# Kernel optimization log

Measured on AMD Instinct MI355X. Metric: run time of the kernel, lower is better.

## Reference

```python
import jax, jax.numpy as jnp
import numpy as np
import math

ALPHA = 2.0  # spikingjelly surrogate.ATan default alpha
TAU = 2.0
MEM_DECAY = math.exp(-1.0 / TAU)
ADAPT_STRENGTH = 0.1
TARGET_RATE = 0.02
THR_MIN = 0.5
N_HEAD = 4

@jax.custom_vjp
def spike_fn(x):
    # Heaviside forward, ATan surrogate backward
    return (x >= 0.0).astype(x.dtype)

def _spike_fwd(x):
    return spike_fn(x), x

def _spike_bwd(x, g):
    return (g * (ALPHA / 2.0) / (1.0 + (jnp.pi / 2.0 * ALPHA * x) ** 2),)

spike_fn.defvjp(_spike_fwd, _spike_bwd)

def lif_step(x, v_mem, thr):
    # thr is a buffer in torch (updated under no_grad): no grad flows to it
    thr_c = jax.lax.stop_gradient(thr)
    v_pot = v_mem * MEM_DECAY + x
    spike = spike_fn(v_pot - thr_c)
    v_new = v_pot * (1.0 - jax.lax.stop_gradient(spike))
    err = jax.lax.stop_gradient(jnp.mean(spike)) - TARGET_RATE
    thr_new = jnp.maximum(thr_c + ADAPT_STRENGTH * err, THR_MIN)
    return spike, v_new, thr_new

def setup_inputs() -> dict:
    key = jax.random.key(0)
    ks = jax.random.split(key, 10)
    B, T, S, D, DS = 8, 16, 256, 512, 64
    x = jax.random.normal(ks[0], (B, T, S, D), jnp.float32)
    A = jax.random.normal(ks[1], (DS, DS), jnp.float32)
    C = jax.random.normal(ks[2], (D, DS), jnp.float32)
    s = 1.0 / math.sqrt(DS)
    Wq = jax.random.uniform(ks[3], (DS, DS), jnp.float32, -s, s)
    bq = jax.random.uniform(ks[4], (DS,), jnp.float32, -s, s)
    sd = 1.0 / math.sqrt(D)
    Wkv = jax.random.uniform(ks[5], (2 * DS, D), jnp.float32, -sd, sd)
    bkv = jax.random.uniform(ks[6], (2 * DS,), jnp.float32, -sd, sd)
    Wo = jax.random.uniform(ks[7], (DS, DS), jnp.float32, -s, s)
    bo = jax.random.uniform(ks[8], (DS,), jnp.float32, -s, s)
    thr_s0 = jnp.full((DS,), 1.0, jnp.float32)
    thr_o0 = jnp.full((D,), 1.0, jnp.float32)
    return {"x": x, "A": A, "C": C, "Wq": Wq, "bq": bq, "Wkv": Wkv,
            "bkv": bkv, "Wo": Wo, "bo": bo, "thr_s0": thr_s0, "thr_o0": thr_o0}

def reference(x, A, C, Wq, bq, Wkv, bkv, Wo, bo, thr_s0, thr_o0):
    B, T, S, D = x.shape
    DS = A.shape[0]
    H = N_HEAD
    dh = DS // H
    N = B * S
    scale = 1.0 / math.sqrt(dh)
    h0 = jnp.zeros((B, S, DS), x.dtype)
    sv0 = jnp.zeros((B, S, DS), x.dtype)
    ov0 = jnp.zeros((B, S, D), x.dtype)

    def step(carry, x_t):
        h, sv, ov, ts, to = carry
        state_transition = h @ A.T                              # (B,S,DS)
        q = (h @ Wq.T + bq).reshape(N, H, dh).transpose(1, 0, 2)   # (H,N,dh)
        kv = x_t @ Wkv.T + bkv                                  # (B,S,2*DS)
        k = kv[..., :DS].reshape(N, H, dh).transpose(1, 0, 2)   # (H,N,dh)
        v = kv[..., DS:].reshape(N, H, dh).transpose(1, 0, 2)   # (H,N,dh)
        scores = jnp.einsum('hnd,hmd->hnm', q, k) * scale       # (H,N,N)
        w = jax.nn.softmax(scores, axis=-1)
        att = jnp.einsum('hnm,hmd->hnd', w, v)                  # (H,N,dh)
        att = att.transpose(1, 0, 2).reshape(B, S, DS)
        state_update = state_transition + att @ Wo.T + bo
        h2, sv2, ts2 = lif_step(state_update, sv, ts)
        output_potential = h2 @ C.T                             # (B,S,D)
        out, ov2, to2 = lif_step(output_potential, ov, to)
        return (h2, sv2, ov2, ts2, to2), out

    _, outs = jax.lax.scan(step, (h0, sv0, ov0, thr_s0, thr_o0),
                           jnp.moveaxis(x, 1, 0))               # outs: (T,B,S,D)
    return jnp.moveaxis(outs, 0, 1)                             # (B,T,S,D)
```

## Files before the change

### kernel.cpp

```cpp
#include <hip/hip_runtime.h>
#include <math.h>


#define NTOK   2048
#define TSTEPS 16
#define NSPLIT 32

#define MEMDECAY ((float)0.6065306597126334)
#define SCALE    0.25f
#define LOG2E    1.4426950408889634f

#define OFF_KV   ((size_t)0)
#define OFF_PACC ((size_t)4194304)
#define OFF_OV   ((size_t)8388608)
#define OFF_H    ((size_t)9437184)
#define OFF_SV   ((size_t)9568256)
#define OFF_Q    ((size_t)9699328)
#define OFF_PM   ((size_t)9830400)
#define OFF_PL   ((size_t)10092544)
#define OFF_CT   ((size_t)10354688)
#define OFF_CNT  ((size_t)10387456)
#define OFF_WT   ((size_t)10387488)
#define OFF_HM   ((size_t)10453024)

__global__ __launch_bounds__(256) void init_kernel(const float* __restrict__ bq,
                                                   const float* __restrict__ C,
                                                   const float* __restrict__ Wkv,
                                                   float* __restrict__ ws) {
  int i = blockIdx.x * 256 + threadIdx.x;
  if (i < 327680) {
    float4 z = {0.f, 0.f, 0.f, 0.f};
    ((float4*)(ws + OFF_OV))[i] = z;
    return;
  }
  i -= 327680;
  if (i < 131072) { ws[OFF_Q + i] = bq[i & 63]; return; }
  i -= 131072;
  if (i < 32768) {
    int k = i >> 9, c = i & 511;
    ws[OFF_CT + i] = C[c * 64 + k];
    return;
  }
  i -= 32768;
  if (i < 65536) {
    int k = i >> 7, o = i & 127;
    ws[OFF_WT + i] = Wkv[o * 512 + k];
    return;
  }
  i -= 65536;
  if (i < 32) { ((int*)(ws + OFF_CNT))[i] = 0; return; }
  i -= 32;
  if (i < 1024) {
    float4 z = {0.f, 0.f, 0.f, 0.f};
    ((float4*)(ws + OFF_HM))[i] = z;
  }
}

__global__ __launch_bounds__(256) void kv_gemm_kernel(const float* __restrict__ x,
                                                      const float* __restrict__ wkt,
                                                      const float* __restrict__ bkv,
                                                      float* __restrict__ ws) {
  __shared__ float xs[64 * 68];
  __shared__ float wt[64 * 136];
  const int tid = threadIdx.x;
  const int mbase = blockIdx.x * 64;
  const int rg = tid >> 4;
  const int cg = tid & 15;

  float acc[4][8];
#pragma unroll
  for (int i = 0; i < 4; ++i)
#pragma unroll
    for (int j = 0; j < 8; ++j) acc[i][j] = 0.f;

  for (int kt = 0; kt < 8; ++kt) {
    const int kb = kt * 64;
#pragma unroll
    for (int p = 0; p < 4; ++p) {
      int e = tid + p * 256;
      int r = e >> 4, kq = e & 15;
      int row = mbase + r;
      int t_ = row >> 11, n = row & 2047;
      int b = n >> 8, s = n & 255;
      float4 v = *(const float4*)(x + (size_t)((b * 16 + t_) * 256 + s) * 512 + kb + kq * 4);
      *(float4*)(xs + r * 68 + kq * 4) = v;
    }
#pragma unroll
    for (int p = 0; p < 8; ++p) {
      int e = tid + p * 256;
      int k = e >> 5, cq = e & 31;
      float4 v = *(const float4*)(wkt + (size_t)(kb + k) * 128 + cq * 4);
      *(float4*)(wt + k * 136 + cq * 4) = v;
    }
    __syncthreads();
#pragma unroll 2
    for (int kq = 0; kq < 16; ++kq) {
      float4 a0 = *(const float4*)(xs + (rg * 4 + 0) * 68 + kq * 4);
      float4 a1 = *(const float4*)(xs + (rg * 4 + 1) * 68 + kq * 4);
      float4 a2 = *(const float4*)(xs + (rg * 4 + 2) * 68 + kq * 4);
      float4 a3 = *(const float4*)(xs + (rg * 4 + 3) * 68 + kq * 4);
      const float* ap[4] = {(const float*)&a0, (const float*)&a1,
                            (const float*)&a2, (const float*)&a3};
#pragma unroll
      for (int kk = 0; kk < 4; ++kk) {
        const float* wp = wt + (kq * 4 + kk) * 136;
        float4 b0 = *(const float4*)(wp + cg * 4);
        float4 b1 = *(const float4*)(wp + 64 + cg * 4);
#pragma unroll
        for (int i = 0; i < 4; ++i) {
          float av = ap[i][kk];
          acc[i][0] += av * b0.x; acc[i][1] += av * b0.y;
          acc[i][2] += av * b0.z; acc[i][3] += av * b0.w;
          acc[i][4] += av * b1.x; acc[i][5] += av * b1.y;
          acc[i][6] += av * b1.z; acc[i][7] += av * b1.w;
        }
      }
    }
    __syncthreads();
  }
  float4 bb0 = *(const float4*)(bkv + cg * 4);
  float4 bb1 = *(const float4*)(bkv + 64 + cg * 4);
  float* kvout = ws + OFF_KV;
#pragma unroll
  for (int i = 0; i < 4; ++i) {
    float* op = kvout + (size_t)(mbase + rg * 4 + i) * 128;
    float4 v0; v0.x = acc[i][0] + bb0.x; v0.y = acc[i][1] + bb0.y;
    v0.z = acc[i][2] + bb0.z; v0.w = acc[i][3] + bb0.w;
    float4 v1; v1.x = acc[i][4] + bb1.x; v1.y = acc[i][5] + bb1.y;
    v1.z = acc[i][6] + bb1.z; v1.w = acc[i][7] + bb1.w;
    *(float4*)(op + cg * 4) = v0;
    *(float4*)(op + 64 + cg * 4) = v1;
  }
}

__device__ __forceinline__ void attp_body(int blk, int tid, int t,
                                          const float* __restrict__ kvbase,
                                          const float* __restrict__ qbuf,
                                          float* __restrict__ pm,
                                          float* __restrict__ pl,
                                          float* __restrict__ pacc,
                                          float* smem) {
  const int head = blk & 3;
  const int qt = (blk >> 2) & 3;
  const int sp = blk >> 4;
  float* kl = smem;
  float* vl = smem + 1024;
  const float* kvt = kvbase + (size_t)t * NTOK * 128;
  {
    int key = tid >> 2, dq = tid & 3;
    const float* base = kvt + (size_t)(sp * 64 + key) * 128 + head * 16;
    float4 kk = ((const float4*)base)[dq];
    float4 vv = ((const float4*)(base + 64))[dq];
    ((float4*)kl)[key * 4 + dq] = kk;
    ((float4*)vl)[key * 4 + dq] = vv;
  }
  const int i0 = qt * 512 + tid;
  const int i1 = i0 + 256;
  float q0[16], q1[16];
  {
    const float4* qp0 = (const float4*)(qbuf + (size_t)i0 * 64 + head * 16);
    const float4* qp1 = (const float4*)(qbuf + (size_t)i1 * 64 + head * 16);
#pragma unroll
    for (int r = 0; r < 4; ++r) {
      float4 a = qp0[r];
      q0[4 * r] = a.x; q0[4 * r + 1] = a.y; q0[4 * r + 2] = a.z; q0[4 * r + 3] = a.w;
      float4 b = qp1[r];
      q1[4 * r] = b.x; q1[4 * r + 1] = b.y; q1[4 * r + 2] = b.z; q1[4 * r + 3] = b.w;
    }
  }
  __syncthreads();
  float m0 = -INFINITY, l0 = 0.f, m1 = -INFINITY, l1 = 0.f;
  float acc0[16], acc1[16];
#pragma unroll
  for (int d = 0; d < 16; ++d) { acc0[d] = 0.f; acc1[d] = 0.f; }

#pragma unroll
  for (int ch = 0; ch < 4; ++ch) {
    float sc0[16], sc1[16];
#pragma unroll
    for (int j = 0; j < 16; ++j) {
      const float* kp = kl + (ch * 16 + j) * 16;
      float s0 = 0.f, s1 = 0.f;
#pragma unroll
      for (int d = 0; d < 16; ++d) { float kv_ = kp[d]; s0 += q0[d] * kv_; s1 += q1[d] * kv_; }
      sc0[j] = s0 * SCALE; sc1[j] = s1 * SCALE;
    }
    float mb0 = sc0[0], mb1 = sc1[0];
#pragma unroll
    for (int j = 1; j < 16; ++j) { mb0 = fmaxf(mb0, sc0[j]); mb1 = fmaxf(mb1, sc1[j]); }
    float mn0 = fmaxf(m0, mb0), mn1 = fmaxf(m1, mb1);
    float r0 = exp2f((m0 - mn0) * LOG2E), r1 = exp2f((m1 - mn1) * LOG2E);
    l0 *= r0; l1 *= r1;
#pragma unroll
    for (int d = 0; d < 16; ++d) { acc0[d] *= r0; acc1[d] *= r1; }
#pragma unroll
    for (int j = 0; j < 16; ++j) {
      float w0 = exp2f((sc0[j] - mn0) * LOG2E), w1 = exp2f((sc1[j] - mn1) * LOG2E);
      l0 += w0; l1 += w1; sc0[j] = w0; sc1[j] = w1;
    }
#pragma unroll
    for (int j = 0; j < 16; ++j) {
      const float* vp = vl + (ch * 16 + j) * 16;
      float w0 = sc0[j], w1 = sc1[j];
#pragma unroll
      for (int d = 0; d < 16; ++d) { float vv = vp[d]; acc0[d] += w0 * vv; acc1[d] += w1 * vv; }
    }
    m0 = mn0; m1 = mn1;
  }
  const int pbase = (head * NSPLIT + sp) * NTOK;
  pm[pbase + i0] = m0; pm[pbase + i1] = m1;
  pl[pbase + i0] = l0; pl[pbase + i1] = l1;
  float4* pa0 = (float4*)(pacc + (size_t)(pbase + i0) * 16);
  float4* pa1 = (float4*)(pacc + (size_t)(pbase + i1) * 16);
#pragma unroll
  for (int r = 0; r < 4; ++r) {
    float4 v0; v0.x = acc0[4 * r]; v0.y = acc0[4 * r + 1]; v0.z = acc0[4 * r + 2]; v0.w = acc0[4 * r + 3];
    pa0[r] = v0;
    float4 v1; v1.x = acc1[4 * r]; v1.y = acc1[4 * r + 1]; v1.z = acc1[4 * r + 2]; v1.w = acc1[4 * r + 3];
    pa1[r] = v1;
  }
}

__global__ __launch_bounds__(256) void attp_kernel(int t, float* __restrict__ ws) {
  __shared__ float smem[2048];
  attp_body(blockIdx.x, threadIdx.x, t, ws + OFF_KV, ws + OFF_Q,
            ws + OFF_PM, ws + OFF_PL, ws + OFF_PACC, smem);
}

__global__ __launch_bounds__(256) void combine_lifs_kernel(
    int t, const float* __restrict__ A, const float* __restrict__ Wq,
    const float* __restrict__ bq, const float* __restrict__ Wo,
    const float* __restrict__ bo, const float* __restrict__ thr_s0,
    float* __restrict__ ws) {
  __shared__ float As[64 * 68], Wqs[64 * 68], Wos[64 * 68];
  __shared__ float att_s[4][64];
  __shared__ int scnt;
  const int tid = threadIdx.x;
#pragma unroll
  for (int p = 0; p < 4; ++p) {
    int e = tid + p * 256;
    int c = e >> 4, kq = e & 15;
    *(float4*)(As + c * 68 + kq * 4)  = *(const float4*)(A + c * 64 + kq * 4);
    *(float4*)(Wqs + c * 68 + kq * 4) = *(const float4*)(Wq + c * 64 + kq * 4);
    *(float4*)(Wos + c * 68 + kq * 4) = *(const float4*)(Wo + c * 64 + kq * 4);
  }
  if (tid == 0) scnt = 0;

  const float* pm = ws + OFF_PM;
  const float* pl = ws + OFF_PL;
  const float* pacc = ws + OFF_PACC;
  float* sv = ws + OFF_SV;
  float* qb = ws + OFF_Q;
  int* cnt = (int*)(ws + OFF_CNT);
  unsigned long long* hmask = (unsigned long long*)(ws + OFF_HM);

  const int lane = tid & 63, w = tid >> 6;
  const int n = blockIdx.x * 4 + w;
  const int head = lane >> 4, d = lane & 15;
  const int pb = head * NSPLIT * NTOK + n;

  float mstar = -INFINITY;
  for (int s = 0; s < NSPLIT; ++s) mstar = fmaxf(mstar, pm[pb + s * NTOK]);
  float lst = 0.f, av = 0.f;
  for (int s = 0; s < NSPLIT; ++s) {
    float e = exp2f((pm[pb + s * NTOK] - mstar) * LOG2E);
    lst += e * pl[pb + s * NTOK];
    av += e * pacc[(size_t)(pb + s * NTOK) * 16 + d];
  }
  att_s[w][lane] = av / lst;
  unsigned long long hm = hmask[n];
  __syncthreads();

  float st = 0.f;
  {
    unsigned long long m = hm;
    while (m) {
      int k = __builtin_ctzll(m);
      m &= m - 1;
      st += As[lane * 68 + k];
    }
  }
  const float* Wor = Wos + lane * 68;
  float wo = 0.f;
#pragma unroll
  for (int kq = 0; kq < 16; ++kq) {
    float4 wb = *(const float4*)(Wor + kq * 4);
    float4 ab = *(const float4*)(&att_s[w][kq * 4]);
    wo += ab.x * wb.x; wo += ab.y * wb.y; wo += ab.z * wb.z; wo += ab.w * wb.w;
  }
  float su = st + wo + bo[lane];

  float thr = thr_s0[0];
  const float inv = 1.0f / 131072.0f;
  for (int i = 0; i < t; ++i) {
    float mean = (float)cnt[i] * inv;
    thr = fmaxf(thr + 0.1f * (mean - 0.02f), 0.5f);
  }
  float svo = sv[n * 64 + lane];
  float vpot = svo * MEMDECAY + su;
  float spk = (vpot >= thr) ? 1.f : 0.f;
  sv[n * 64 + lane] = vpot * (1.f - spk);
  unsigned long long sm = __ballot(spk > 0.5f);

  float qv = 0.f;
  {
    unsigned long long m = sm;
    while (m) {
      int k = __builtin_ctzll(m);
      m &= m - 1;
      qv += Wqs[lane * 68 + k];
    }
  }
  qb[n * 64 + lane] = qv + bq[lane];

  if (lane == 0) {
    hmask[n] = sm;
    atomicAdd(&scnt, __popcll(sm));
  }
  __syncthreads();
  if (tid == 0) atomicAdd(&cnt[t], scnt);
}

__global__ __launch_bounds__(256) void fused_out_attp_kernel(
    int t, const float* __restrict__ thr_o0, float* __restrict__ out,
    float* __restrict__ ws) {
  __shared__ float smem[2048];
  __shared__ int scnt;
  const int blk = blockIdx.x;
  if (blk >= 256) {
    attp_body(blk - 256, threadIdx.x, t + 1, ws + OFF_KV, ws + OFF_Q,
              ws + OFF_PM, ws + OFF_PL, ws + OFF_PACC, smem);
    return;
  }
  const int tid = threadIdx.x;
  const int nt = blk >> 3;
  const int ct = blk & 7;
  const float* Ct = ws + OFF_CT;
  float* ov = ws + OFF_OV;
  int* cnt = (int*)(ws + OFF_CNT);
  const unsigned long long* hmask = (const unsigned long long*)(ws + OFF_HM);

  if (tid == 0) scnt = 0;
  __syncthreads();

  const int tr = tid >> 4, tc = tid & 15;
  float thr = thr_o0[0];
  const float inv = 1.0f / 1048576.0f;
  for (int i = 0; i < t; ++i) {
    float mean = (float)cnt[16 + i] * inv;
    thr = fmaxf(thr + 0.1f * (mean - 0.02f), 0.5f);
  }

  int mycount = 0;
#pragma unroll
  for (int i = 0; i < 4; ++i) {
    int n = nt * 64 + tr + i * 16;
    size_t coff = (size_t)ct * 64 + tc * 4;
    float a0 = 0.f, a1 = 0.f, a2 = 0.f, a3 = 0.f;
    unsigned long long m = hmask[n];
    while (m) {
      int k = __builtin_ctzll(m);
      m &= m - 1;
      float4 c = *(const float4*)(Ct + (size_t)k * 512 + coff);
      a0 += c.x; a1 += c.y; a2 += c.z; a3 += c.w;
    }
    int b = n >> 8, s = n & 255;
    float* ovp = ov + (size_t)n * 512 + coff;
    float* outp = out + ((size_t)(b * 16 + t) * 256 + s) * 512 + coff;
    float4 o = *(float4*)ovp;
    float v0 = o.x * MEMDECAY + a0;
    float v1 = o.y * MEMDECAY + a1;
    float v2 = o.z * MEMDECAY + a2;
    float v3 = o.w * MEMDECAY + a3;
    float s0 = (v0 >= thr) ? 1.f : 0.f;
    float s1 = (v1 >= thr) ? 1.f : 0.f;
    float s2 = (v2 >= thr) ? 1.f : 0.f;
    float s3 = (v3 >= thr) ? 1.f : 0.f;
    float4 sp; sp.x = s0; sp.y = s1; sp.z = s2; sp.w = s3;
    *(float4*)outp = sp;
    float4 nv; nv.x = v0 * (1.f - s0); nv.y = v1 * (1.f - s1);
    nv.z = v2 * (1.f - s2); nv.w = v3 * (1.f - s3);
    *(float4*)ovp = nv;
    mycount += (int)(s0 + s1 + s2 + s3);
  }
  atomicAdd(&scnt, mycount);
  __syncthreads();
  if (tid == 0) atomicAdd(&cnt[16 + t], scnt);
}

extern "C" void kernel_launch(void* const* d_in, const int* in_sizes, int n_in,
                              void* d_out, int out_size, void* d_ws, size_t ws_size,
                              hipStream_t stream) {
  const float* x    = (const float*)d_in[0];
  const float* A    = (const float*)d_in[1];
  const float* C    = (const float*)d_in[2];
  const float* Wq   = (const float*)d_in[3];
  const float* bq   = (const float*)d_in[4];
  const float* Wkv  = (const float*)d_in[5];
  const float* bkv  = (const float*)d_in[6];
  const float* Wo   = (const float*)d_in[7];
  const float* bo   = (const float*)d_in[8];
  const float* th_s = (const float*)d_in[9];
  const float* th_o = (const float*)d_in[10];
  float* out = (float*)d_out;
  float* ws = (float*)d_ws;

  init_kernel<<<dim3(2181), dim3(256), 0, stream>>>(bq, C, Wkv, ws);
  kv_gemm_kernel<<<dim3(512), dim3(256), 0, stream>>>(x, ws + OFF_WT, bkv, ws);
  attp_kernel<<<dim3(512), dim3(256), 0, stream>>>(0, ws);
  for (int t = 0; t < TSTEPS; ++t) {
    combine_lifs_kernel<<<dim3(512), dim3(256), 0, stream>>>(t, A, Wq, bq, Wo, bo, th_s, ws);
    int g = (t < TSTEPS - 1) ? 768 : 256;
    fused_out_attp_kernel<<<dim3(g), dim3(256), 0, stream>>>(t, th_o, out, ws);
  }
}
```

Baseline: 910.3 us.

## Broadcast K/V via readlane registers instead of LDS; read A/Wq rows from global

In the attention partial kernel, each lane now holds one key's K and V slice in registers, and the values are broadcast with readlane inside the score and accumulation loops. This replaces the shared-memory staging and its barrier. The chunk loop is no longer fully unrolled, which lowers register pressure. In combine_lifs, the A and Wq tiles are no longer copied into LDS; the sparse spike-indexed sums read them straight from global/L1. This cuts LDS use and staging work, but adds readlane scalar traffic and uncoalesced global reads.

```diff
diff --git a/kernel.cpp b/kernel.cpp
--- a/kernel.cpp
+++ b/kernel.cpp
@@ -10,10 +10,13 @@
 #define SCALE    0.25f
 #define LOG2E    1.4426950408889634f
 
+__device__ __forceinline__ float rdlane(float v, int j) {
+  return __int_as_float(__builtin_amdgcn_readlane(__float_as_int(v), j));
+}
+
 #define OFF_KV   ((size_t)0)
 #define OFF_PACC ((size_t)4194304)
 #define OFF_OV   ((size_t)8388608)
-#define OFF_H    ((size_t)9437184)
 #define OFF_SV   ((size_t)9568256)
 #define OFF_Q    ((size_t)9699328)
 #define OFF_PM   ((size_t)9830400)
@@ -138,22 +141,12 @@
                                           const float* __restrict__ qbuf,
                                           float* __restrict__ pm,
                                           float* __restrict__ pl,
-                                          float* __restrict__ pacc,
-                                          float* smem) {
+                                          float* __restrict__ pacc) {
   const int head = blk & 3;
   const int qt = (blk >> 2) & 3;
   const int sp = blk >> 4;
-  float* kl = smem;
-  float* vl = smem + 1024;
+  const int lane = tid & 63;
   const float* kvt = kvbase + (size_t)t * NTOK * 128;
-  {
-    int key = tid >> 2, dq = tid & 3;
-    const float* base = kvt + (size_t)(sp * 64 + key) * 128 + head * 16;
-    float4 kk = ((const float4*)base)[dq];
-    float4 vv = ((const float4*)(base + 64))[dq];
-    ((float4*)kl)[key * 4 + dq] = kk;
-    ((float4*)vl)[key * 4 + dq] = vv;
-  }
   const int i0 = qt * 512 + tid;
   const int i1 = i0 + 256;
   float q0[16], q1[16];
@@ -168,42 +161,57 @@
       q1[4 * r] = b.x; q1[4 * r + 1] = b.y; q1[4 * r + 2] = b.z; q1[4 * r + 3] = b.w;
     }
   }
-  __syncthreads();
+  float Kd[16], Vd[16];
+  {
+    const float* kp = kvt + (size_t)(sp * 64 + lane) * 128 + head * 16;
+#pragma unroll
+    for (int xx = 0; xx < 4; ++xx) {
+      float4 kk = ((const float4*)kp)[xx];
+      Kd[4 * xx] = kk.x; Kd[4 * xx + 1] = kk.y; Kd[4 * xx + 2] = kk.z; Kd[4 * xx + 3] = kk.w;
+      float4 vv = ((const float4*)(kp + 64))[xx];
+      Vd[4 * xx] = vv.x; Vd[4 * xx + 1] = vv.y; Vd[4 * xx + 2] = vv.z; Vd[4 * xx + 3] = vv.w;
+    }
+  }
   float m0 = -INFINITY, l0 = 0.f, m1 = -INFINITY, l1 = 0.f;
   float acc0[16], acc1[16];
 #pragma unroll
   for (int d = 0; d < 16; ++d) { acc0[d] = 0.f; acc1[d] = 0.f; }
 
-#pragma unroll
   for (int ch = 0; ch < 4; ++ch) {
     float sc0[16], sc1[16];
-#pragma unroll
-    for (int j = 0; j < 16; ++j) {
-      const float* kp = kl + (ch * 16 + j) * 16;
+#pragma unroll 4
+    for (int jj = 0; jj < 16; ++jj) {
+      const int j = ch * 16 + jj;
       float s0 = 0.f, s1 = 0.f;
 #pragma unroll
-      for (int d = 0; d < 16; ++d) { float kv_ = kp[d]; s0 += q0[d] * kv_; s1 += q1[d] * kv_; }
-      sc0[j] = s0 * SCALE; sc1[j] = s1 * SCALE;
+      for (int d = 0; d < 16; ++d) {
+        float kd = rdlane(Kd[d], j);
+        s0 += q0[d] * kd; s1 += q1[d] * kd;
+      }
+      sc0[jj] = s0 * SCALE; sc1[jj] = s1 * SCALE;
     }
     float mb0 = sc0[0], mb1 = sc1[0];
 #pragma unroll
-    for (int j = 1; j < 16; ++j) { mb0 = fmaxf(mb0, sc0[j]); mb1 = fmaxf(mb1, sc1[j]); }
+    for (int jj = 1; jj < 16; ++jj) { mb0 = fmaxf(mb0, sc0[jj]); mb1 = fmaxf(mb1, sc1[jj]); }
     float mn0 = fmaxf(m0, mb0), mn1 = fmaxf(m1, mb1);
     float r0 = exp2f((m0 - mn0) * LOG2E), r1 = exp2f((m1 - mn1) * LOG2E);
     l0 *= r0; l1 *= r1;
 #pragma unroll
     for (int d = 0; d < 16; ++d) { acc0[d] *= r0; acc1[d] *= r1; }
 #pragma unroll
-    for (int j = 0; j < 16; ++j) {
-      float w0 = exp2f((sc0[j] - mn0) * LOG2E), w1 = exp2f((sc1[j] - mn1) * LOG2E);
-      l0 += w0; l1 += w1; sc0[j] = w0; sc1[j] = w1;
-    }
-#pragma unroll
-    for (int j = 0; j < 16; ++j) {
-      const float* vp = vl + (ch * 16 + j) * 16;
-      float w0 = sc0[j], w1 = sc1[j];
-#pragma unroll
-      for (int d = 0; d < 16; ++d) { float vv = vp[d]; acc0[d] += w0 * vv; acc1[d] += w1 * vv; }
+    for (int jj = 0; jj < 16; ++jj) {
+      float w0 = exp2f((sc0[jj] - mn0) * LOG2E), w1 = exp2f((sc1[jj] - mn1) * LOG2E);
+      l0 += w0; l1 += w1; sc0[jj] = w0; sc1[jj] = w1;
+    }
+#pragma unroll 4
+    for (int jj = 0; jj < 16; ++jj) {
+      const int j = ch * 16 + jj;
+      float w0 = sc0[jj], w1 = sc1[jj];
+#pragma unroll
+      for (int d = 0; d < 16; ++d) {
+        float vd = rdlane(Vd[d], j);
+        acc0[d] += w0 * vd; acc1[d] += w1 * vd;
+      }
     }
     m0 = mn0; m1 = mn1;
   }
@@ -222,9 +230,8 @@
 }
 
 __global__ __launch_bounds__(256) void attp_kernel(int t, float* __restrict__ ws) {
-  __shared__ float smem[2048];
   attp_body(blockIdx.x, threadIdx.x, t, ws + OFF_KV, ws + OFF_Q,
-            ws + OFF_PM, ws + OFF_PL, ws + OFF_PACC, smem);
+            ws + OFF_PM, ws + OFF_PL, ws + OFF_PACC);
 }
 
 __global__ __launch_bounds__(256) void combine_lifs_kernel(
@@ -232,7 +239,7 @@
     const float* __restrict__ bq, const float* __restrict__ Wo,
     const float* __restrict__ bo, const float* __restrict__ thr_s0,
     float* __restrict__ ws) {
-  __shared__ float As[64 * 68], Wqs[64 * 68], Wos[64 * 68];
+  __shared__ float Wos[64 * 68];
   __shared__ float att_s[4][64];
   __shared__ int scnt;
   const int tid = threadIdx.x;
@@ -240,8 +247,6 @@
   for (int p = 0; p < 4; ++p) {
     int e = tid + p * 256;
     int c = e >> 4, kq = e & 15;
-    *(float4*)(As + c * 68 + kq * 4)  = *(const float4*)(A + c * 64 + kq * 4);
-    *(float4*)(Wqs + c * 68 + kq * 4) = *(const float4*)(Wq + c * 64 + kq * 4);
     *(float4*)(Wos + c * 68 + kq * 4) = *(const float4*)(Wo + c * 64 + kq * 4);
   }
   if (tid == 0) scnt = 0;
@@ -269,7 +274,6 @@
   }
   att_s[w][lane] = av / lst;
   unsigned long long hm = hmask[n];
-  __syncthreads();
 
   float st = 0.f;
   {
@@ -277,9 +281,11 @@
     while (m) {
       int k = __builtin_ctzll(m);
       m &= m - 1;
-      st += As[lane * 68 + k];
-    }
-  }
+      st += A[lane * 64 + k];
+    }
+  }
+  __syncthreads();
+
   const float* Wor = Wos + lane * 68;
   float wo = 0.f;
 #pragma unroll
@@ -308,7 +314,7 @@
     while (m) {
       int k = __builtin_ctzll(m);
       m &= m - 1;
-      qv += Wqs[lane * 68 + k];
+      qv += Wq[lane * 64 + k];
     }
   }
   qb[n * 64 + lane] = qv + bq[lane];
@@ -324,12 +330,11 @@
 __global__ __launch_bounds__(256) void fused_out_attp_kernel(
     int t, const float* __restrict__ thr_o0, float* __restrict__ out,
     float* __restrict__ ws) {
-  __shared__ float smem[2048];
   __shared__ int scnt;
   const int blk = blockIdx.x;
   if (blk >= 256) {
     attp_body(blk - 256, threadIdx.x, t + 1, ws + OFF_KV, ws + OFF_Q,
-              ws + OFF_PM, ws + OFF_PL, ws + OFF_PACC, smem);
+              ws + OFF_PM, ws + OFF_PL, ws + OFF_PACC);
     return;
   }
   const int tid = threadIdx.x;
```

Result: slower. 1.170 ms (+28.5%).
